# Performance work log

Measured on AMD Instinct MI355X. Metric: run time of the kernel, lower is better.

## Reference

```python
import jax, jax.numpy as jnp
import numpy as np

NUM_HEADS = 8


def setup_inputs() -> dict:
    key = jax.random.key(0)
    k1, k2, k3, k4 = jax.random.split(key, 4)
    E = 256
    seq = jax.random.normal(k1, (4, 256, E, 16, 16), dtype=jnp.float32)
    W_qkv = jax.random.normal(k2, (3 * E, E), dtype=jnp.float32) * (E ** -0.5)
    W_out = jax.random.normal(k3, (E, E), dtype=jnp.float32) * (E ** -0.5)
    b_out = jax.random.normal(k4, (E,), dtype=jnp.float32)
    return {"seq": seq, "W_qkv": W_qkv, "W_out": W_out, "b_out": b_out,
            "n_sub_x": 16, "n_sub_y": 16}


def reference(seq, W_qkv, W_out, b_out, n_sub_x, n_sub_y):
    # seq: [b, s, c, h, w] -- a sequence of functions (tokens on spatial grids)
    b, s, c, h, w = seq.shape
    H = NUM_HEADS
    d = c // H  # head_dim

    # pointwise QKV projection along the channel axis (no bias)
    qkv = jnp.einsum('oc,bscxy->bsoxy', W_qkv, seq)  # [b, s, 3c, h, w]
    # channel layout per einops: (num_heads, split=3, head_dim)
    qkv = qkv.reshape(b, s, H, 3, d, h, w)
    qkv = jnp.transpose(qkv, (3, 0, 2, 1, 4, 5, 6))  # [3, b, H, s, d, h, w]
    q, k, v = qkv[0], qkv[1], qkv[2]

    # func_attention: L2 inner product over head_dim and spatial dims
    scale = 1.0 / np.sqrt(d * h * w).astype(np.float32)
    scores = jnp.einsum('bhqdxy,bhkdxy->bhqk', q, k) * scale  # [b, H, s, s]
    attn = jax.nn.softmax(scores, axis=-1)
    sa = jnp.einsum('bhqk,bhkdxy->bhqdxy', attn, v)  # [b, H, s, d, h, w]

    # merge heads back to channel axis: 'b h s d ... -> b s (h d) ...'
    sa = jnp.transpose(sa, (0, 2, 1, 3, 4, 5)).reshape(b, s, c, h, w)

    # output projection (with bias) along channels
    out = jnp.einsum('oc,bscxy->bsoxy', W_out, sa)
    out = out + b_out[None, None, :, None, None]
    return out
```

## Files before the change

kernel.cpp:

```cpp
#include <hip/hip_runtime.h>
#include <stdint.h>


#define DI __device__ __forceinline__

typedef __attribute__((ext_vector_type(4))) float  f32x4;
typedef __attribute__((ext_vector_type(8))) short  s16x8;
typedef __attribute__((ext_vector_type(4))) short  s16x4;
typedef __attribute__((ext_vector_type(8))) __bf16 bf16x8;

DI unsigned short f2bf(float f) {
    unsigned int u = __builtin_bit_cast(unsigned int, f);
    u = (u + 0x7fffu + ((u >> 16) & 1u)) >> 16;
    return (unsigned short)u;
}
DI bf16x8 asbf(s16x8 v) { return __builtin_bit_cast(bf16x8, v); }
#define MFMA16(a, b, c) __builtin_amdgcn_mfma_f32_16x16x32_bf16((a), (b), (c), 0, 0, 0)

#define GLOAD16(g, l) __builtin_amdgcn_global_load_lds( \
    (const __attribute__((address_space(1))) unsigned int*)(g), \
    (__attribute__((address_space(3))) unsigned int*)(l), 16, 0, 0)


DI void sgk_loadA(const unsigned short* __restrict__ Asrc,
                  s16x8 af[4][8], int wm, int lg, int lr) {
#pragma unroll
    for (int m = 0; m < 4; m++)
#pragma unroll
        for (int kf = 0; kf < 8; kf++)
            af[m][kf] = *(const s16x8*)(Asrc + (size_t)(wm + m * 16 + lr) * 256
                                        + kf * 32 + lg * 8);
}

DI void sgk_stage(const unsigned short* src, size_t rstride,
                  unsigned short* lds, int tid) {
#pragma unroll
    for (int i = 0; i < 8; i++)
        GLOAD16(src + (size_t)(i * 8) * rstride, lds + ((i * 256 + tid) << 3));
}

DI void sgk_mfma(const unsigned short* __restrict__ Bl,
                 const s16x8 af[4][8], f32x4 acc[4][4], int lg, int lr) {
    const f32x4 z4 = {0.f, 0.f, 0.f, 0.f};
    {
        s16x8 bfv[4];
#pragma unroll
        for (int n = 0; n < 4; n++)
            bfv[n] = *(const s16x8*)&Bl[(n * 16 + lr) * 256 + ((lg ^ (lr & 7)) << 3)];
#pragma unroll
        for (int n = 0; n < 4; n++) {
            bf16x8 bv = asbf(bfv[n]);
#pragma unroll
            for (int m = 0; m < 4; m++)
                acc[m][n] = MFMA16(asbf(af[m][0]), bv, z4);
        }
    }
#pragma unroll
    for (int kf = 1; kf < 8; kf++) {
        s16x8 bfv[4];
#pragma unroll
        for (int n = 0; n < 4; n++)
            bfv[n] = *(const s16x8*)&Bl[(n * 16 + lr) * 256
                                        + (((kf * 4 + lg) ^ (lr & 7)) << 3)];
#pragma unroll
        for (int n = 0; n < 4; n++) {
            bf16x8 bv = asbf(bfv[n]);
#pragma unroll
            for (int m = 0; m < 4; m++)
                acc[m][n] = MFMA16(asbf(af[m][kf]), bv, acc[m][n]);
        }
    }
}

#define SGK_SETUP()                                           \
    const int tid = threadIdx.x, ln = tid & 63, w = tid >> 6; \
    const int wm = w * 64;                                    \
    const int lg = ln >> 4, lr = ln & 15;                     \
    const size_t swoff = (size_t)(((tid & 31) ^ ((tid >> 5) & 7)) * 8); \
    const size_t srow = (size_t)(tid >> 5);

__global__ __launch_bounds__(64) void k_prep(
    const float* __restrict__ Wqkv, const float* __restrict__ Wout,
    unsigned short* __restrict__ Wbf)
{
    int r = blockIdx.x, ln = threadIdx.x;
    const float* src;
    if (r < 768) {
        int split = r >> 8, hd = r & 255;
        src = Wqkv + (size_t)(((hd >> 5) * 96) + split * 32 + (hd & 31)) * 256;
    } else {
        src = Wout + (size_t)(r - 768) * 256;
    }
    f32x4 v = *(const f32x4*)(src + ln * 4);
    s16x4 h = {(short)f2bf(v.x), (short)f2bf(v.y), (short)f2bf(v.z), (short)f2bf(v.w)};
    *(s16x4*)&Wbf[(size_t)r * 256 + ln * 4] = h;
}

__global__ __launch_bounds__(256) void k_tr(
    const float* __restrict__ seq, unsigned short* __restrict__ seqT)
{
    const int bs = blockIdx.x, tid = threadIdx.x;
    __shared__ __align__(16) unsigned short T[64][264];
    const float* src = seq + (size_t)bs * 65536;
    unsigned short* dst = seqT + (size_t)bs * 65536;

    for (int co = 0; co < 256; co += 64) {
        {
            int r = tid >> 2, p0 = (tid & 3) * 64;
            const float* s = src + (size_t)(co + r) * 256 + p0;
#pragma unroll
            for (int i = 0; i < 8; i++) {
                f32x4 a = *(const f32x4*)(s + i * 8);
                f32x4 b = *(const f32x4*)(s + i * 8 + 4);
                s16x8 h = {(short)f2bf(a.x), (short)f2bf(a.y), (short)f2bf(a.z),
                           (short)f2bf(a.w), (short)f2bf(b.x), (short)f2bf(b.y),
                           (short)f2bf(b.z), (short)f2bf(b.w)};
                *(s16x8*)&T[r][p0 + i * 8] = h;
            }
        }
        __syncthreads();
        {
            unsigned short e[64];
#pragma unroll
            for (int c = 0; c < 64; c++) e[c] = T[c][tid];
            unsigned short* d = dst + (size_t)tid * 256 + co;
#pragma unroll
            for (int j = 0; j < 8; j++) {
                s16x8 v = {(short)e[j * 8 + 0], (short)e[j * 8 + 1],
                           (short)e[j * 8 + 2], (short)e[j * 8 + 3],
                           (short)e[j * 8 + 4], (short)e[j * 8 + 5],
                           (short)e[j * 8 + 6], (short)e[j * 8 + 7]};
                *(s16x8*)(d + j * 8) = v;
            }
        }
        __syncthreads();
    }
}

__global__ __launch_bounds__(256, 2) void k_qkT(
    const unsigned short* __restrict__ seqT, const unsigned short* __restrict__ Wbf,
    unsigned short* __restrict__ Qb, unsigned short* __restrict__ Kb)
{
    const int mt = blockIdx.x >> 8, g = blockIdx.x & 255;

    __shared__ __align__(16) unsigned short Bb[2][16384];

    SGK_SETUP();

    s16x8 af[4][8];
    sgk_loadA(Wbf + (size_t)mt * 65536, af, wm, lg, lr);

    const unsigned short* Bsrc = seqT + (size_t)g * 262144 + srow * 256 + swoff;
    unsigned short* const dstB = mt ? Kb : Qb;

    sgk_stage(Bsrc, 256, Bb[0], tid);
    __syncthreads();

    for (int t = 0; t < 16; t++) {
        if (t + 1 < 16)
            sgk_stage(Bsrc + (size_t)(t + 1) * 16384, 256, Bb[(t + 1) & 1], tid);
        f32x4 acc[4][4];
        sgk_mfma(Bb[t & 1], af, acc, lg, lr);
        __syncthreads();

        const int bs = g * 4 + (t >> 2);
        const int b = bs >> 8, s = bs & 255;
        const int pb = (t & 3) * 64;
#pragma unroll
        for (int m = 0; m < 4; m++) {
#pragma unroll
            for (int rr = 0; rr < 4; rr++) {
                int oo = wm + m * 16 + lg * 4 + rr;
                size_t base = ((size_t)((b * 8 + (oo >> 5)) * 256 + s)) * 8192
                            + (size_t)(oo & 31) * 256 + pb + lr;
#pragma unroll
                for (int n = 0; n < 4; n++)
                    dstB[base + n * 16] = f2bf(acc[m][n][rr]);
            }
        }
    }
}

__global__ __launch_bounds__(256, 2) void k_vT(
    const unsigned short* __restrict__ seqT, const unsigned short* __restrict__ Wbf,
    unsigned short* __restrict__ Vt)
{
    const int b = blockIdx.x >> 7, pg = blockIdx.x & 127;

    __shared__ __align__(16) unsigned short Bb[2][16384];

    SGK_SETUP();

    s16x8 af[4][8];
    sgk_loadA(Wbf + 131072, af, wm, lg, lr);

    const unsigned short* Bsrc = seqT + ((size_t)b * 256 + srow) * 65536 + swoff;

#define VT_TILE(t) (Bsrc + (size_t)(pg * 2 + ((t) >> 2)) * 256 \
                         + (size_t)(((t) & 3) * 64) * 65536)

    sgk_stage(VT_TILE(0), 65536, Bb[0], tid);
    __syncthreads();

    for (int t = 0; t < 8; t++) {
        if (t + 1 < 8)
            sgk_stage(VT_TILE(t + 1), 65536, Bb[(t + 1) & 1], tid);
        f32x4 acc[4][4];
        sgk_mfma(Bb[t & 1], af, acc, lg, lr);
        __syncthreads();

        const int p = pg * 2 + (t >> 2);
        const int sb = (t & 3) * 64;
#pragma unroll
        for (int m = 0; m < 4; m++) {
#pragma unroll
            for (int rr = 0; rr < 4; rr++) {
                int o = wm + m * 16 + lg * 4 + rr;
                size_t base = (size_t)(b * 8 + (o >> 5)) * 2097152
                            + (size_t)(p * 32 + (o & 31)) * 256 + sb + lr;
#pragma unroll
                for (int n = 0; n < 4; n++)
                    Vt[base + n * 16] = f2bf(acc[m][n][rr]);
            }
        }
    }
#undef VT_TILE
}

__global__ __launch_bounds__(256, 2) void k_avT(
    const unsigned short* __restrict__ Pb, const unsigned short* __restrict__ Vt,
    unsigned short* __restrict__ SAT)
{
    const int bh = blockIdx.x >> 4, nsl = blockIdx.x & 15;
    const int b = bh >> 3, h = bh & 7;

    __shared__ __align__(16) unsigned short Bb[2][16384];

    SGK_SETUP();

    s16x8 af[4][8];
    sgk_loadA(Pb + (size_t)bh * 65536, af, wm, lg, lr);

    const unsigned short* Bsrc = Vt + (size_t)bh * 2097152
                               + (size_t)(nsl * 512) * 256 + srow * 256 + swoff;

    sgk_stage(Bsrc, 256, Bb[0], tid);
    __syncthreads();

    for (int t = 0; t < 8; t++) {
        if (t + 1 < 8)
            sgk_stage(Bsrc + (size_t)(t + 1) * 16384, 256, Bb[(t + 1) & 1], tid);
        f32x4 acc[4][4];
        sgk_mfma(Bb[t & 1], af, acc, lg, lr);
        __syncthreads();

        const int fb = nsl * 512 + t * 64;
#pragma unroll
        for (int m = 0; m < 4; m++) {
#pragma unroll
            for (int rr = 0; rr < 4; rr++) {
                int q = wm + m * 16 + lg * 4 + rr;
                size_t qb = (size_t)(b * 256 + q) * 65536;
#pragma unroll
                for (int n = 0; n < 4; n++) {
                    int p = (fb + n * 16) >> 5;
                    int clo = ((fb + n * 16) & 31);
                    SAT[qb + (size_t)p * 256 + h * 32 + clo + lr] = f2bf(acc[m][n][rr]);
                }
            }
        }
    }
}

__global__ __launch_bounds__(256, 2) void k_outT(
    const unsigned short* __restrict__ SAT, const unsigned short* __restrict__ Wbf,
    const float* __restrict__ bias, float* __restrict__ out)
{
    const int g = blockIdx.x;

    __shared__ __align__(16) unsigned short Bb[2][16384];

    SGK_SETUP();

    s16x8 af[4][8];
    sgk_loadA(Wbf + 196608, af, wm, lg, lr);

    float bo[4][4];
#pragma unroll
    for (int m = 0; m < 4; m++)
#pragma unroll
        for (int rr = 0; rr < 4; rr++)
            bo[m][rr] = bias[wm + m * 16 + lg * 4 + rr];

    const unsigned short* Bsrc = SAT + (size_t)g * 131072 + srow * 256 + swoff;

    sgk_stage(Bsrc, 256, Bb[0], tid);
    __syncthreads();

    for (int t = 0; t < 8; t++) {
        if (t + 1 < 8)
            sgk_stage(Bsrc + (size_t)(t + 1) * 16384, 256, Bb[(t + 1) & 1], tid);
        f32x4 acc[4][4];
        sgk_mfma(Bb[t & 1], af, acc, lg, lr);
        __syncthreads();

        const int bs = g * 2 + (t >> 2);
        const int pb = (t & 3) * 64;
#pragma unroll
        for (int m = 0; m < 4; m++) {
#pragma unroll
            for (int rr = 0; rr < 4; rr++) {
                int o = wm + m * 16 + lg * 4 + rr;
                float* d = out + ((size_t)bs * 256 + o) * 256 + pb + lr;
#pragma unroll
                for (int n = 0; n < 4; n++)
                    d[n * 16] = acc[m][n][rr] + bo[m][rr];
            }
        }
    }
}

DI void cls_stage(const unsigned short* gp, size_t stride,
                  unsigned short* lbase, int w) {
#pragma unroll
    for (int i = 0; i < 4; i++)
        GLOAD16(gp + (size_t)(i * 8) * stride, lbase + (w * 4 + i) * 512);
}

DI void cls_mfma(const unsigned short* __restrict__ Al,
                 const unsigned short* __restrict__ Bl,
                 f32x4 acc[4][4], int wm, int wn, int lg, int lr) {
#pragma unroll
    for (int kk = 0; kk < 2; kk++) {
        int off = (((kk * 4 + lg) ^ (lr & 7)) << 3);
        s16x8 af[4];
#pragma unroll
        for (int m = 0; m < 4; m++)
            af[m] = *(const s16x8*)&Al[(wm + m * 16 + lr) * 64 + off];
        s16x8 bf[4];
#pragma unroll
        for (int n = 0; n < 4; n++)
            bf[n] = *(const s16x8*)&Bl[(wn + n * 16 + lr) * 64 + off];
#pragma unroll
        for (int n = 0; n < 4; n++) {
            bf16x8 bv = asbf(bf[n]);
#pragma unroll
            for (int m = 0; m < 4; m++)
                acc[m][n] = MFMA16(asbf(af[m]), bv, acc[m][n]);
        }
    }
}

__global__ __launch_bounds__(256, 2) void k_scores(
    const unsigned short* __restrict__ Qb, const unsigned short* __restrict__ Kb,
    float* __restrict__ Sp)
{
    const int bh = blockIdx.y;
    const int kc = blockIdx.x & 3, st = (blockIdx.x >> 2) & 1, mt = blockIdx.x >> 3;
    const int tid = threadIdx.x, ln = tid & 63, w = tid >> 6;
    const int wm = (w >> 1) * 64, wn = (w & 1) * 64;
    const int lg = ln >> 4, lr = ln & 15;
    const int srow = ln >> 3;
    const int schk = (ln & 7) ^ srow;

    __shared__ __align__(16) unsigned short Ab[2][8192];
    __shared__ __align__(16) unsigned short Bb[2][8192];

    f32x4 acc[4][4];
    const f32x4 z4 = {0.f, 0.f, 0.f, 0.f};
#pragma unroll
    for (int m = 0; m < 4; m++)
#pragma unroll
        for (int n = 0; n < 4; n++) acc[m][n] = z4;

    const unsigned short* gA = Qb + (size_t)(bh * 256 + mt * 128 + w * 32 + srow) * 8192
                             + kc * 2048 + schk * 8;
    const unsigned short* gB = Kb + (size_t)(bh * 256 + st * 128 + w * 32 + srow) * 8192
                             + kc * 2048 + schk * 8;

    cls_stage(gA, 8192, Ab[0], w);
    cls_stage(gB, 8192, Bb[0], w);
    __syncthreads();
    for (int t = 0; t < 32; t++) {
        if (t + 1 < 32) {
            cls_stage(gA + (size_t)(t + 1) * 64, 8192, Ab[(t + 1) & 1], w);
            cls_stage(gB + (size_t)(t + 1) * 64, 8192, Bb[(t + 1) & 1], w);
        }
        cls_mfma(Ab[t & 1], Bb[t & 1], acc, wm, wn, lg, lr);
        __syncthreads();
    }

    float* dst = Sp + (size_t)kc * 2097152
               + (size_t)(bh * 256 + mt * 128 + wm) * 256 + st * 128 + wn;
#pragma unroll
    for (int m = 0; m < 4; m++) {
#pragma unroll
        for (int rr = 0; rr < 4; rr++) {
            float* d = dst + (size_t)(m * 16 + lg * 4 + rr) * 256 + lr;
#pragma unroll
            for (int n = 0; n < 4; n++)
                d[n * 16] = acc[m][n][rr];
        }
    }
}

__global__ __launch_bounds__(256) void k_softmax(
    const float* __restrict__ Sp, unsigned short* __restrict__ Pb)
{
    const int tid = threadIdx.x, ln = tid & 63;
    const int row = blockIdx.x * 4 + (tid >> 6);
    const float scale = 0.011048543456039806f;

    const float* p0 = Sp + (size_t)row * 256 + ln * 4;
    f32x4 v = *(const f32x4*)p0;
#pragma unroll
    for (int k = 1; k < 4; k++)
        v += *(const f32x4*)(p0 + (size_t)k * 2097152);
    v *= scale;

    float m = fmaxf(fmaxf(v.x, v.y), fmaxf(v.z, v.w));
#pragma unroll
    for (int off = 32; off; off >>= 1) m = fmaxf(m, __shfl_xor(m, off));
    float e0 = __expf(v.x - m), e1 = __expf(v.y - m);
    float e2 = __expf(v.z - m), e3 = __expf(v.w - m);
    float sum = e0 + e1 + e2 + e3;
#pragma unroll
    for (int off = 32; off; off >>= 1) sum += __shfl_xor(sum, off);
    float inv = 1.f / sum;
    s16x4 p = {(short)f2bf(e0 * inv), (short)f2bf(e1 * inv),
               (short)f2bf(e2 * inv), (short)f2bf(e3 * inv)};
    *(s16x4*)(Pb + (size_t)row * 256 + ln * 4) = p;
}

extern "C" void kernel_launch(void* const* d_in, const int* in_sizes, int n_in,
                              void* d_out, int out_size, void* d_ws, size_t ws_size,
                              hipStream_t stream)
{
    const float* seq  = (const float*)d_in[0];
    const float* Wqkv = (const float*)d_in[1];
    const float* Wout = (const float*)d_in[2];
    const float* bout = (const float*)d_in[3];

    unsigned short* Qb = (unsigned short*)d_out;
    unsigned short* Kb = Qb + 67108864;

    unsigned short* Vt   = (unsigned short*)d_ws;
    unsigned short* seqT = Vt + 67108864;
    float*          Sp   = (float*)seqT;
    unsigned short* SAT  = seqT;
    unsigned short* Pb   = (unsigned short*)d_ws + 134217728;
    unsigned short* Wbf  = Pb + 2097152;

    float* out = (float*)d_out;

    k_prep<<<dim3(1024), dim3(64), 0, stream>>>(Wqkv, Wout, Wbf);
    k_tr<<<dim3(1024), dim3(256), 0, stream>>>(seq, seqT);
    k_qkT<<<dim3(512), dim3(256), 0, stream>>>(seqT, Wbf, Qb, Kb);
    k_vT<<<dim3(512), dim3(256), 0, stream>>>(seqT, Wbf, Vt);
    k_scores<<<dim3(16, 32), dim3(256), 0, stream>>>(Qb, Kb, Sp);
    k_softmax<<<dim3(2048), dim3(256), 0, stream>>>(Sp, Pb);
    k_avT<<<dim3(512), dim3(256), 0, stream>>>(Pb, Vt, SAT);
    k_outT<<<dim3(512), dim3(256), 0, stream>>>(SAT, Wbf, bout, out);
}
```

Measured before the change: 552.8 us.

## Fuse softmax into AV kernel and overlap LDS staging with split waitcnt barriers

Replaces the __syncthreads around the double-buffered global-to-LDS staging in all GEMM kernels with explicit vmcnt waits plus raw barriers and sched barriers. The intent is to let the next tile's loads stay in flight while the current tile is computed. Separately, the standalone softmax kernel is removed: k_avT now reduces the split-K partial scores, applies the softmax and packs the probabilities to bf16 directly in registers. This saves a launch and the Pb round trip, at the cost of every AV block recomputing the softmax for its rows (16x redundancy across nsl slices). Sp moves to a separate workspace region.

```diff
diff --git a/kernel.cpp b/kernel.cpp
--- a/kernel.cpp
+++ b/kernel.cpp
@@ -20,6 +20,11 @@
 #define GLOAD16(g, l) __builtin_amdgcn_global_load_lds( \
     (const __attribute__((address_space(1))) unsigned int*)(g), \
     (__attribute__((address_space(3))) unsigned int*)(l), 16, 0, 0)
+
+#define WAIT_VM8() asm volatile("s_waitcnt vmcnt(8)" ::: "memory")
+#define WAIT_VM0() asm volatile("s_waitcnt vmcnt(0)" ::: "memory")
+#define BAR()    __builtin_amdgcn_s_barrier()
+#define SCHED0() __builtin_amdgcn_sched_barrier(0)
 
 
 DI void sgk_loadA(const unsigned short* __restrict__ Asrc,
@@ -154,14 +159,17 @@
     unsigned short* const dstB = mt ? Kb : Qb;
 
     sgk_stage(Bsrc, 256, Bb[0], tid);
-    __syncthreads();
 
     for (int t = 0; t < 16; t++) {
-        if (t + 1 < 16)
+        if (t + 1 < 16) {
             sgk_stage(Bsrc + (size_t)(t + 1) * 16384, 256, Bb[(t + 1) & 1], tid);
+            WAIT_VM8();
+        } else {
+            WAIT_VM0();
+        }
+        BAR(); SCHED0();
         f32x4 acc[4][4];
         sgk_mfma(Bb[t & 1], af, acc, lg, lr);
-        __syncthreads();
 
         const int bs = g * 4 + (t >> 2);
         const int b = bs >> 8, s = bs & 255;
@@ -178,6 +186,7 @@
                     dstB[base + n * 16] = f2bf(acc[m][n][rr]);
             }
         }
+        SCHED0(); BAR();
     }
 }
 
@@ -200,14 +209,17 @@
                          + (size_t)(((t) & 3) * 64) * 65536)
 
     sgk_stage(VT_TILE(0), 65536, Bb[0], tid);
-    __syncthreads();
 
     for (int t = 0; t < 8; t++) {
-        if (t + 1 < 8)
+        if (t + 1 < 8) {
             sgk_stage(VT_TILE(t + 1), 65536, Bb[(t + 1) & 1], tid);
+            WAIT_VM8();
+        } else {
+            WAIT_VM0();
+        }
+        BAR(); SCHED0();
         f32x4 acc[4][4];
         sgk_mfma(Bb[t & 1], af, acc, lg, lr);
-        __syncthreads();
 
         const int p = pg * 2 + (t >> 2);
         const int sb = (t & 3) * 64;
@@ -223,12 +235,13 @@
                     Vt[base + n * 16] = f2bf(acc[m][n][rr]);
             }
         }
+        SCHED0(); BAR();
     }
 #undef VT_TILE
 }
 
 __global__ __launch_bounds__(256, 2) void k_avT(
-    const unsigned short* __restrict__ Pb, const unsigned short* __restrict__ Vt,
+    const float* __restrict__ Sp, const unsigned short* __restrict__ Vt,
     unsigned short* __restrict__ SAT)
 {
     const int bh = blockIdx.x >> 4, nsl = blockIdx.x & 15;
@@ -238,21 +251,73 @@
 
     SGK_SETUP();
 
-    s16x8 af[4][8];
-    sgk_loadA(Pb + (size_t)bh * 65536, af, wm, lg, lr);
-
     const unsigned short* Bsrc = Vt + (size_t)bh * 2097152
                                + (size_t)(nsl * 512) * 256 + srow * 256 + swoff;
-
     sgk_stage(Bsrc, 256, Bb[0], tid);
-    __syncthreads();
+
+    s16x8 af[4][8];
+    {
+        const float scale = 0.011048543456039806f;
+        const float* sp0 = Sp + (size_t)bh * 65536 + lg * 8;
+#pragma unroll
+        for (int m = 0; m < 4; m++) {
+            int q = wm + m * 16 + lr;
+            const float* rp = sp0 + (size_t)q * 256;
+            f32x4 v0[8], v1[8];
+#pragma unroll
+            for (int kf = 0; kf < 8; kf++) {
+                f32x4 a = *(const f32x4*)(rp + kf * 32);
+                f32x4 c = *(const f32x4*)(rp + kf * 32 + 4);
+#pragma unroll
+                for (int kc = 1; kc < 4; kc++) {
+                    a += *(const f32x4*)(rp + (size_t)kc * 2097152 + kf * 32);
+                    c += *(const f32x4*)(rp + (size_t)kc * 2097152 + kf * 32 + 4);
+                }
+                v0[kf] = a * scale;
+                v1[kf] = c * scale;
+            }
+            float mx = -1e30f;
+#pragma unroll
+            for (int kf = 0; kf < 8; kf++) {
+                mx = fmaxf(mx, fmaxf(fmaxf(v0[kf].x, v0[kf].y), fmaxf(v0[kf].z, v0[kf].w)));
+                mx = fmaxf(mx, fmaxf(fmaxf(v1[kf].x, v1[kf].y), fmaxf(v1[kf].z, v1[kf].w)));
+            }
+            mx = fmaxf(mx, __shfl_xor(mx, 16));
+            mx = fmaxf(mx, __shfl_xor(mx, 32));
+            float sm = 0.f;
+#pragma unroll
+            for (int kf = 0; kf < 8; kf++) {
+                v0[kf].x = __expf(v0[kf].x - mx); v0[kf].y = __expf(v0[kf].y - mx);
+                v0[kf].z = __expf(v0[kf].z - mx); v0[kf].w = __expf(v0[kf].w - mx);
+                v1[kf].x = __expf(v1[kf].x - mx); v1[kf].y = __expf(v1[kf].y - mx);
+                v1[kf].z = __expf(v1[kf].z - mx); v1[kf].w = __expf(v1[kf].w - mx);
+                sm += (v0[kf].x + v0[kf].y + v0[kf].z + v0[kf].w)
+                    + (v1[kf].x + v1[kf].y + v1[kf].z + v1[kf].w);
+            }
+            sm += __shfl_xor(sm, 16);
+            sm += __shfl_xor(sm, 32);
+            float inv = 1.f / sm;
+#pragma unroll
+            for (int kf = 0; kf < 8; kf++) {
+                s16x8 pk = {(short)f2bf(v0[kf].x * inv), (short)f2bf(v0[kf].y * inv),
+                            (short)f2bf(v0[kf].z * inv), (short)f2bf(v0[kf].w * inv),
+                            (short)f2bf(v1[kf].x * inv), (short)f2bf(v1[kf].y * inv),
+                            (short)f2bf(v1[kf].z * inv), (short)f2bf(v1[kf].w * inv)};
+                af[m][kf] = pk;
+            }
+        }
+    }
 
     for (int t = 0; t < 8; t++) {
-        if (t + 1 < 8)
+        if (t + 1 < 8) {
             sgk_stage(Bsrc + (size_t)(t + 1) * 16384, 256, Bb[(t + 1) & 1], tid);
+            WAIT_VM8();
+        } else {
+            WAIT_VM0();
+        }
+        BAR(); SCHED0();
         f32x4 acc[4][4];
         sgk_mfma(Bb[t & 1], af, acc, lg, lr);
-        __syncthreads();
 
         const int fb = nsl * 512 + t * 64;
 #pragma unroll
@@ -269,6 +334,7 @@
                 }
             }
         }
+        SCHED0(); BAR();
     }
 }
 
@@ -295,14 +361,17 @@
     const unsigned short* Bsrc = SAT + (size_t)g * 131072 + srow * 256 + swoff;
 
     sgk_stage(Bsrc, 256, Bb[0], tid);
-    __syncthreads();
 
     for (int t = 0; t < 8; t++) {
-        if (t + 1 < 8)
+        if (t + 1 < 8) {
             sgk_stage(Bsrc + (size_t)(t + 1) * 16384, 256, Bb[(t + 1) & 1], tid);
+            WAIT_VM8();
+        } else {
+            WAIT_VM0();
+        }
+        BAR(); SCHED0();
         f32x4 acc[4][4];
         sgk_mfma(Bb[t & 1], af, acc, lg, lr);
-        __syncthreads();
 
         const int bs = g * 2 + (t >> 2);
         const int pb = (t & 3) * 64;
@@ -317,6 +386,7 @@
                     d[n * 16] = acc[m][n][rr] + bo[m][rr];
             }
         }
+        SCHED0(); BAR();
     }
 }
 
@@ -380,14 +450,18 @@
 
     cls_stage(gA, 8192, Ab[0], w);
     cls_stage(gB, 8192, Bb[0], w);
-    __syncthreads();
+
     for (int t = 0; t < 32; t++) {
         if (t + 1 < 32) {
             cls_stage(gA + (size_t)(t + 1) * 64, 8192, Ab[(t + 1) & 1], w);
             cls_stage(gB + (size_t)(t + 1) * 64, 8192, Bb[(t + 1) & 1], w);
-        }
+            WAIT_VM8();
+        } else {
+            WAIT_VM0();
+        }
+        BAR(); SCHED0();
         cls_mfma(Ab[t & 1], Bb[t & 1], acc, wm, wn, lg, lr);
-        __syncthreads();
+        SCHED0(); BAR();
     }
 
     float* dst = Sp + (size_t)kc * 2097152
@@ -402,34 +476,6 @@
                 d[n * 16] = acc[m][n][rr];
         }
     }
-}
-
-__global__ __launch_bounds__(256) void k_softmax(
-    const float* __restrict__ Sp, unsigned short* __restrict__ Pb)
-{
-    const int tid = threadIdx.x, ln = tid & 63;
-    const int row = blockIdx.x * 4 + (tid >> 6);
-    const float scale = 0.011048543456039806f;
-
-    const float* p0 = Sp + (size_t)row * 256 + ln * 4;
-    f32x4 v = *(const f32x4*)p0;
-#pragma unroll
-    for (int k = 1; k < 4; k++)
-        v += *(const f32x4*)(p0 + (size_t)k * 2097152);
-    v *= scale;
-
-    float m = fmaxf(fmaxf(v.x, v.y), fmaxf(v.z, v.w));
-#pragma unroll
-    for (int off = 32; off; off >>= 1) m = fmaxf(m, __shfl_xor(m, off));
-    float e0 = __expf(v.x - m), e1 = __expf(v.y - m);
-    float e2 = __expf(v.z - m), e3 = __expf(v.w - m);
-    float sum = e0 + e1 + e2 + e3;
-#pragma unroll
-    for (int off = 32; off; off >>= 1) sum += __shfl_xor(sum, off);
-    float inv = 1.f / sum;
-    s16x4 p = {(short)f2bf(e0 * inv), (short)f2bf(e1 * inv),
-               (short)f2bf(e2 * inv), (short)f2bf(e3 * inv)};
-    *(s16x4*)(Pb + (size_t)row * 256 + ln * 4) = p;
 }
 
 extern "C" void kernel_launch(void* const* d_in, const int* in_sizes, int n_in,
@@ -446,10 +492,9 @@
 
     unsigned short* Vt   = (unsigned short*)d_ws;
     unsigned short* seqT = Vt + 67108864;
-    float*          Sp   = (float*)seqT;
     unsigned short* SAT  = seqT;
-    unsigned short* Pb   = (unsigned short*)d_ws + 134217728;
-    unsigned short* Wbf  = Pb + 2097152;
+    float*          Sp   = (float*)(seqT + 67108864);
+    unsigned short* Wbf  = (unsigned short*)(Sp + 8388608);
 
     float* out = (float*)d_out;
 
@@ -458,7 +503,6 @@
     k_qkT<<<dim3(512), dim3(256), 0, stream>>>(seqT, Wbf, Qb, Kb);
     k_vT<<<dim3(512), dim3(256), 0, stream>>>(seqT, Wbf, Vt);
     k_scores<<<dim3(16, 32), dim3(256), 0, stream>>>(Qb, Kb, Sp);
-    k_softmax<<<dim3(2048), dim3(256), 0, stream>>>(Sp, Pb);
-    k_avT<<<dim3(512), dim3(256), 0, stream>>>(Pb, Vt, SAT);
+    k_avT<<<dim3(512), dim3(256), 0, stream>>>(Sp, Vt, SAT);
     k_outT<<<dim3(512), dim3(256), 0, stream>>>(SAT, Wbf, bout, out);
 }
```

After: 631.0 us. 1.14x slower.

## Permute intermediate layouts so epilogue stores pack into vector writes

Applied to the files above, without the earlier changes.

The QKV projection epilogue now writes its four bf16 outputs per row as one 8-byte store, and the attention-output epilogue writes pairs as 32-bit stores, instead of scattering 2-byte stores. This permutes the element order inside the intermediate buffers. To compensate, the prep kernel permutes the columns of the output-projection weights to match the new SAT channel order. The change targets many narrow uncoalesced global stores, but it depends on every downstream consumer (including k_vT and the attention kernels, whose code is only partly visible) being consistent with the permuted orders.

```diff
diff --git a/kernel.cpp b/kernel.cpp
--- a/kernel.cpp
+++ b/kernel.cpp
@@ -84,16 +84,27 @@
     unsigned short* __restrict__ Wbf)
 {
     int r = blockIdx.x, ln = threadIdx.x;
-    const float* src;
     if (r < 768) {
         int split = r >> 8, hd = r & 255;
-        src = Wqkv + (size_t)(((hd >> 5) * 96) + split * 32 + (hd & 31)) * 256;
+        const float* src = Wqkv + (size_t)(((hd >> 5) * 96) + split * 32 + (hd & 31)) * 256;
+        f32x4 v = *(const f32x4*)(src + ln * 4);
+        s16x4 h = {(short)f2bf(v.x), (short)f2bf(v.y), (short)f2bf(v.z), (short)f2bf(v.w)};
+        *(s16x4*)&Wbf[(size_t)r * 256 + ln * 4] = h;
     } else {
-        src = Wout + (size_t)(r - 768) * 256;
-    }
-    f32x4 v = *(const f32x4*)(src + ln * 4);
-    s16x4 h = {(short)f2bf(v.x), (short)f2bf(v.y), (short)f2bf(v.z), (short)f2bf(v.w)};
-    *(s16x4*)&Wbf[(size_t)r * 256 + ln * 4] = h;
+        int o = r - 768;
+        const float* src = Wout + (size_t)o * 256;
+        int cp0 = ln * 4;
+        int hh = cp0 >> 5;
+        unsigned short vals[4];
+#pragma unroll
+        for (int j = 0; j < 4; j++) {
+            int jj = (cp0 + j) & 31;
+            int dd = (jj >> 1) + ((jj & 1) << 4);
+            vals[j] = f2bf(src[hh * 32 + dd]);
+        }
+        s16x4 h4 = {(short)vals[0], (short)vals[1], (short)vals[2], (short)vals[3]};
+        *(s16x4*)&Wbf[(size_t)r * 256 + cp0] = h4;
+    }
 }
 
 __global__ __launch_bounds__(256) void k_tr(
@@ -172,10 +183,10 @@
             for (int rr = 0; rr < 4; rr++) {
                 int oo = wm + m * 16 + lg * 4 + rr;
                 size_t base = ((size_t)((b * 8 + (oo >> 5)) * 256 + s)) * 8192
-                            + (size_t)(oo & 31) * 256 + pb + lr;
-#pragma unroll
-                for (int n = 0; n < 4; n++)
-                    dstB[base + n * 16] = f2bf(acc[m][n][rr]);
+                            + (size_t)(oo & 31) * 256 + pb + lr * 4;
+                s16x4 pk = {(short)f2bf(acc[m][0][rr]), (short)f2bf(acc[m][1][rr]),
+                            (short)f2bf(acc[m][2][rr]), (short)f2bf(acc[m][3][rr])};
+                *(s16x4*)(dstB + base) = pk;
             }
         }
     }
@@ -255,18 +266,20 @@
         __syncthreads();
 
         const int fb = nsl * 512 + t * 64;
+        const int p0 = fb >> 5;
 #pragma unroll
         for (int m = 0; m < 4; m++) {
 #pragma unroll
             for (int rr = 0; rr < 4; rr++) {
                 int q = wm + m * 16 + lg * 4 + rr;
-                size_t qb = (size_t)(b * 256 + q) * 65536;
-#pragma unroll
-                for (int n = 0; n < 4; n++) {
-                    int p = (fb + n * 16) >> 5;
-                    int clo = ((fb + n * 16) & 31);
-                    SAT[qb + (size_t)p * 256 + h * 32 + clo + lr] = f2bf(acc[m][n][rr]);
-                }
+                size_t base = (size_t)(b * 256 + q) * 65536
+                            + (size_t)p0 * 256 + h * 32 + lr * 2;
+                unsigned int v01 = (unsigned int)f2bf(acc[m][0][rr])
+                                 | ((unsigned int)f2bf(acc[m][1][rr]) << 16);
+                unsigned int v23 = (unsigned int)f2bf(acc[m][2][rr])
+                                 | ((unsigned int)f2bf(acc[m][3][rr]) << 16);
+                *(unsigned int*)(SAT + base) = v01;
+                *(unsigned int*)(SAT + base + 256) = v23;
             }
         }
     }
```

After: 538.2 us. -2.6%, faster.
